# Performance work log

Hardware: AMD Instinct MI355X
Metric: run time of the kernel (lower is better)

The kernel has to match this reference:

```python
import jax, jax.numpy as jnp
import numpy as np

N_NODES = 1_000_000
MEM_DIM = 128
EDGE_DIM = 64
TIME_DIM = 16
N_EVENTS = 100_000
GRU_IN = 2 * MEM_DIM + EDGE_DIM + TIME_DIM  # 336


def setup_inputs() -> dict:
    key = jax.random.key(0)
    ks = jax.random.split(key, 16)
    sc = 0.05
    return {
        "memory": jax.random.normal(ks[0], (N_NODES, MEM_DIM), jnp.float32),
        "src": jax.random.randint(ks[1], (N_EVENTS,), 0, N_NODES, jnp.int32),
        "dst": jax.random.randint(ks[2], (N_EVENTS,), 0, N_NODES, jnp.int32),
        "ts": jax.random.uniform(ks[3], (N_EVENTS,), jnp.float32),
        "ef": jax.random.normal(ks[4], (N_EVENTS, EDGE_DIM), jnp.float32),
        # time_linear: Linear(1, 16)
        "W_time": jax.random.normal(ks[5], (TIME_DIM, 1), jnp.float32) * sc,
        "b_time": jax.random.normal(ks[6], (TIME_DIM,), jnp.float32) * sc,
        # GRUCell(336, 128): torch layout, gate order (r, z, n)
        "W_ih": jax.random.normal(ks[7], (3 * MEM_DIM, GRU_IN), jnp.float32) * sc,
        "W_hh": jax.random.normal(ks[8], (3 * MEM_DIM, MEM_DIM), jnp.float32) * sc,
        "b_ih": jax.random.normal(ks[9], (3 * MEM_DIM,), jnp.float32) * sc,
        "b_hh": jax.random.normal(ks[10], (3 * MEM_DIM,), jnp.float32) * sc,
        # predictor: Linear(256,128) -> ReLU -> Linear(128,1)
        "W_p1": jax.random.normal(ks[11], (MEM_DIM, 2 * MEM_DIM), jnp.float32) * sc,
        "b_p1": jax.random.normal(ks[12], (MEM_DIM,), jnp.float32) * sc,
        "W_p2": jax.random.normal(ks[13], (1, MEM_DIM), jnp.float32) * sc,
        "b_p2": jax.random.normal(ks[14], (1,), jnp.float32) * sc,
    }


def _gru_cell(x, h, W_ih, W_hh, b_ih, b_hh):
    gi = x @ W_ih.T + b_ih  # [E, 3H]
    gh = h @ W_hh.T + b_hh  # [E, 3H]
    i_r, i_z, i_n = jnp.split(gi, 3, axis=-1)
    h_r, h_z, h_n = jnp.split(gh, 3, axis=-1)
    r = jax.nn.sigmoid(i_r + h_r)
    z = jax.nn.sigmoid(i_z + h_z)
    n = jnp.tanh(i_n + r * h_n)
    return (1.0 - z) * n + z * h


def reference(memory, src, dst, ts, ef, W_time, b_time, W_ih, W_hh, b_ih, b_hh,
              W_p1, b_p1, W_p2, b_p2):
    # update_memory: gather -> time encode -> GRU -> scatter (dst write after src, matching torch)
    s = memory[src]  # [E, H]
    d = memory[dst]  # [E, H]
    te = jnp.sin(ts[:, None] @ W_time.T + b_time)  # [E, 16]
    inp = jnp.concatenate([s, d, ef, te], axis=-1)  # [E, 336]
    new_s = _gru_cell(inp, s, W_ih, W_hh, b_ih, b_hh)
    new_d = _gru_cell(inp, d, W_ih, W_hh, b_ih, b_hh)
    mem = memory.at[src].set(new_s).at[dst].set(new_d)
    # predict on updated memory
    h = jnp.concatenate([mem[src], mem[dst]], axis=-1)  # [E, 2H]
    pred = (jax.nn.relu(h @ W_p1.T + b_p1) @ W_p2.T + b_p2).squeeze(-1)  # [E]
    return pred, mem
```

## Files before the change

### kernel.cpp

```cpp
#include <hip/hip_runtime.h>
#include <hip/hip_bf16.h>
#include <math.h>

static constexpr int NN  = 1000000;
static constexpr int HD  = 128;
static constexpr int ED  = 64;
static constexpr int TD  = 16;
static constexpr int NE  = 100000;
static constexpr int GIN = 336;
static constexpr int KP  = 352;
static constexpr int KS  = KP / 32;
static constexpr int EB  = 32;
static constexpr int PS  = 264;
static constexpr int NBG = NE / EB;
static constexpr int NBC = 2 * NBG;
static constexpr int CR  = NN / NBC;
static constexpr int NIH = 24 * KS * 512;
static constexpr int NHH = 24 * 4 * 512;
static constexpr int NP1 = 8 * 8 * 512;
static constexpr int NBW = (NE + 511) / 512;
static constexpr int NBV = (NIH + NHH + NP1) / 512;

typedef __attribute__((ext_vector_type(8))) short bf16x8;
typedef __attribute__((ext_vector_type(4))) float f32x4;

__device__ inline unsigned f2bf(float x) {
    union { float f; unsigned u; } a; a.f = x;
    unsigned r = a.u + 0x7fff + ((a.u >> 16) & 1);
    return r >> 16;
}
__device__ inline float bf2f(unsigned short u) {
    union { unsigned u; float f; } a; a.u = ((unsigned)u) << 16; return a.f;
}
__device__ inline float fsig(float x) {
    return __builtin_amdgcn_rcpf(1.f + __builtin_amdgcn_exp2f(x * -1.44269504f));
}
__device__ inline float ftanh(float x) {
    return 1.f - 2.f * __builtin_amdgcn_rcpf(1.f + __builtin_amdgcn_exp2f(x * 2.88539008f));
}

__global__ void prio_kernel(const int* __restrict__ src, const int* __restrict__ dst,
                            int* __restrict__ prio) {
    int e = blockIdx.x * blockDim.x + threadIdx.x;
    if (e < NE) {
        atomicMax(&prio[src[e]], e);
        atomicMax(&prio[dst[e]], NE + e);
    }
}

__global__ __launch_bounds__(512) void prep_kernel(
    const float* __restrict__ memory,
    const int* __restrict__ src, const int* __restrict__ dst,
    const float* __restrict__ ts, const float* __restrict__ ef,
    const float* __restrict__ W_time, const float* __restrict__ b_time,
    const float* __restrict__ W_ih, const float* __restrict__ W_hh,
    const float* __restrict__ W_p1,
    const int* __restrict__ prio, unsigned char* __restrict__ win,
    unsigned short* __restrict__ A_pack,
    unsigned short* __restrict__ Wihf, unsigned short* __restrict__ Whhf,
    unsigned short* __restrict__ Wp1f,
    float* __restrict__ mem_out)
{
    const int bid = blockIdx.x;
    const int tid = threadIdx.x;

    if (bid < NBC + NBG) {
        if (bid % 3 != 2) {
            const int cb = (bid / 3) * 2 + (bid % 3);
            const float4* in4  = (const float4*)memory;
            float4*       out4 = (float4*)mem_out;
            const size_t base = (size_t)cb * CR * 32;
            for (int i = tid; i < CR * 32; i += 512)
                out4[base + i] = in4[base + i];
        } else {
            const int e0 = (bid / 3) * EB;
            for (int idx = tid; idx < EB * 88; idx += 512) {
                int e = idx / 88, c4 = idx % 88;
                float4 v = {0.f, 0.f, 0.f, 0.f};
                if (c4 < 32)      v = ((const float4*)&memory[(size_t)src[e0 + e] * HD])[c4];
                else if (c4 < 64) v = ((const float4*)&memory[(size_t)dst[e0 + e] * HD])[c4 - 32];
                else if (c4 < 80) v = ((const float4*)&ef[(size_t)(e0 + e) * ED])[c4 - 64];
                else if (c4 < 84) {
                    int j = (c4 - 80) * 4;
                    float t = ts[e0 + e];
                    v.x = __sinf(t * W_time[j]     + b_time[j]);
                    v.y = __sinf(t * W_time[j + 1] + b_time[j + 1]);
                    v.z = __sinf(t * W_time[j + 2] + b_time[j + 2]);
                    v.w = __sinf(t * W_time[j + 3] + b_time[j + 3]);
                }
                uint2 p;
                p.x = f2bf(v.x) | (f2bf(v.y) << 16);
                p.y = f2bf(v.z) | (f2bf(v.w) << 16);
                *(uint2*)&A_pack[(size_t)(e0 + e) * KP + c4 * 4] = p;
            }
        }
    } else if (bid < NBC + NBG + NBW) {
        int e = (bid - NBC - NBG) * 512 + tid;
        if (e < NE)
            win[e] = (unsigned char)((prio[src[e]] == e ? 1 : 0) |
                                     (prio[dst[e]] == NE + e ? 2 : 0));
    } else {
        int q = (bid - NBC - NBG - NBW) * 512 + tid;
        if (q < NIH) {
            int t = q / (KS * 512), rem = q % (KS * 512);
            int kk = rem / 512, li = rem % 512;
            int l = li >> 3, j = li & 7;
            int row = t * 16 + (l & 15);
            int col = kk * 32 + (l >> 4) * 8 + j;
            Wihf[q] = (col < GIN) ? (unsigned short)f2bf(W_ih[(size_t)row * GIN + col])
                                  : (unsigned short)0;
        } else if (q < NIH + NHH) {
            int p = q - NIH;
            int t = p / (4 * 512), rem = p % (4 * 512);
            int kk = rem / 512, li = rem % 512;
            int l = li >> 3, j = li & 7;
            int row = t * 16 + (l & 15);
            int col = kk * 32 + (l >> 4) * 8 + j;
            Whhf[p] = (unsigned short)f2bf(W_hh[(size_t)row * HD + col]);
        } else {
            int p = q - NIH - NHH;
            int w = p / (8 * 512), rem = p % (8 * 512);
            int kk = rem / 512, li = rem % 512;
            int l = li >> 3, j = li & 7;
            int row = w * 16 + (l & 15);
            int col = kk * 32 + (l >> 4) * 8 + j;
            Wp1f[p] = (unsigned short)f2bf(W_p1[(size_t)row * (2 * HD) + col]);
        }
    }
}

__global__ __launch_bounds__(512) void gru_kernel(
    const unsigned short* __restrict__ A_pack,
    const int* __restrict__ src, const int* __restrict__ dst,
    const unsigned short* __restrict__ Wihf, const unsigned short* __restrict__ Whhf,
    const float* __restrict__ b_ih, const float* __restrict__ b_hh,
    const unsigned char* __restrict__ win, float* __restrict__ mem_out)
{
    __shared__ unsigned short a_lds[EB * KP];
    const int tid = threadIdx.x;
    const int e0  = blockIdx.x * EB;

    {
        const uint4* g4 = (const uint4*)(A_pack + (size_t)e0 * KP);
        uint4* l4 = (uint4*)a_lds;
        for (int i = tid; i < EB * KP / 8; i += 512)
            l4[i] = g4[i];
    }
    __syncthreads();

    const int w    = tid >> 6;
    const int lane = tid & 63;
    const int lg   = lane >> 4;
    const int u    = w * 16 + (lane & 15);
    const int arow = lane & 15;

#define ALD(t, kkk) (*(const bf16x8*)&a_lds[(arow + (t) * 16) * KP + (kkk) * 32 + lg * 8])

    f32x4 z4 = {0.f, 0.f, 0.f, 0.f};
    f32x4 ir0 = z4, ir1 = z4, iz0 = z4, iz1 = z4, in0 = z4, in1 = z4;
    f32x4 sr0 = z4, sr1 = z4, sz0 = z4, sz1 = z4, sn0 = z4, sn1 = z4;
    f32x4 dr0 = z4, dr1 = z4, dz0 = z4, dz1 = z4, dn0 = z4, dn1 = z4;

#pragma unroll
    for (int kk = 0; kk < KS; ++kk) {
        bf16x8 b0 = *(const bf16x8*)&Wihf[(((size_t)(0 * 8 + w) * KS + kk) * 64 + lane) * 8];
        bf16x8 b1 = *(const bf16x8*)&Wihf[(((size_t)(1 * 8 + w) * KS + kk) * 64 + lane) * 8];
        bf16x8 b2 = *(const bf16x8*)&Wihf[(((size_t)(2 * 8 + w) * KS + kk) * 64 + lane) * 8];
        bf16x8 a0 = ALD(0, kk), a1 = ALD(1, kk);
        ir0 = __builtin_amdgcn_mfma_f32_16x16x32_bf16(a0, b0, ir0, 0, 0, 0);
        ir1 = __builtin_amdgcn_mfma_f32_16x16x32_bf16(a1, b0, ir1, 0, 0, 0);
        iz0 = __builtin_amdgcn_mfma_f32_16x16x32_bf16(a0, b1, iz0, 0, 0, 0);
        iz1 = __builtin_amdgcn_mfma_f32_16x16x32_bf16(a1, b1, iz1, 0, 0, 0);
        in0 = __builtin_amdgcn_mfma_f32_16x16x32_bf16(a0, b2, in0, 0, 0, 0);
        in1 = __builtin_amdgcn_mfma_f32_16x16x32_bf16(a1, b2, in1, 0, 0, 0);
    }
#pragma unroll
    for (int kk = 0; kk < 4; ++kk) {
        bf16x8 c0 = *(const bf16x8*)&Whhf[(((size_t)(0 * 8 + w) * 4 + kk) * 64 + lane) * 8];
        bf16x8 c1 = *(const bf16x8*)&Whhf[(((size_t)(1 * 8 + w) * 4 + kk) * 64 + lane) * 8];
        bf16x8 c2 = *(const bf16x8*)&Whhf[(((size_t)(2 * 8 + w) * 4 + kk) * 64 + lane) * 8];
        bf16x8 as0 = ALD(0, kk),     as1 = ALD(1, kk);
        bf16x8 ad0 = ALD(0, kk + 4), ad1 = ALD(1, kk + 4);
        sr0 = __builtin_amdgcn_mfma_f32_16x16x32_bf16(as0, c0, sr0, 0, 0, 0);
        sr1 = __builtin_amdgcn_mfma_f32_16x16x32_bf16(as1, c0, sr1, 0, 0, 0);
        dr0 = __builtin_amdgcn_mfma_f32_16x16x32_bf16(ad0, c0, dr0, 0, 0, 0);
        dr1 = __builtin_amdgcn_mfma_f32_16x16x32_bf16(ad1, c0, dr1, 0, 0, 0);
        sz0 = __builtin_amdgcn_mfma_f32_16x16x32_bf16(as0, c1, sz0, 0, 0, 0);
        sz1 = __builtin_amdgcn_mfma_f32_16x16x32_bf16(as1, c1, sz1, 0, 0, 0);
        dz0 = __builtin_amdgcn_mfma_f32_16x16x32_bf16(ad0, c1, dz0, 0, 0, 0);
        dz1 = __builtin_amdgcn_mfma_f32_16x16x32_bf16(ad1, c1, dz1, 0, 0, 0);
        sn0 = __builtin_amdgcn_mfma_f32_16x16x32_bf16(as0, c2, sn0, 0, 0, 0);
        sn1 = __builtin_amdgcn_mfma_f32_16x16x32_bf16(as1, c2, sn1, 0, 0, 0);
        dn0 = __builtin_amdgcn_mfma_f32_16x16x32_bf16(ad0, c2, dn0, 0, 0, 0);
        dn1 = __builtin_amdgcn_mfma_f32_16x16x32_bf16(ad1, c2, dn1, 0, 0, 0);
    }
#undef ALD

    const float bir = b_ih[u], biz = b_ih[u + 128], bin_ = b_ih[u + 256];
    const float bhr = b_hh[u], bhz = b_hh[u + 128], bhn = b_hh[u + 256];

    auto epilogue = [&](int t, f32x4 ir, f32x4 iz, f32x4 in_,
                        f32x4 sr, f32x4 sz, f32x4 sn,
                        f32x4 dr, f32x4 dz, f32x4 dn) {
#pragma unroll
        for (int j = 0; j < 4; ++j) {
            int el = t * 16 + lg * 4 + j, e = e0 + el;
            unsigned char wf = win[e];
            float gr_ = ir[j] + bir, gz_ = iz[j] + biz, gn_ = in_[j] + bin_;
            if (wf & 1) {
                float r = fsig(gr_ + sr[j] + bhr);
                float z = fsig(gz_ + sz[j] + bhz);
                float n = ftanh(gn_ + r * (sn[j] + bhn));
                float h = bf2f(a_lds[el * KP + u]);
                mem_out[(size_t)src[e] * HD + u] = (1.f - z) * n + z * h;
            }
            if (wf & 2) {
                float r = fsig(gr_ + dr[j] + bhr);
                float z = fsig(gz_ + dz[j] + bhz);
                float n = ftanh(gn_ + r * (dn[j] + bhn));
                float h = bf2f(a_lds[el * KP + 128 + u]);
                mem_out[(size_t)dst[e] * HD + u] = (1.f - z) * n + z * h;
            }
        }
    };
    epilogue(0, ir0, iz0, in0, sr0, sz0, sn0, dr0, dz0, dn0);
    epilogue(1, ir1, iz1, in1, sr1, sz1, sn1, dr1, dz1, dn1);
}

__global__ __launch_bounds__(512) void pred_kernel(
    const float* __restrict__ mem,
    const int* __restrict__ src, const int* __restrict__ dst,
    const unsigned short* __restrict__ Wp1f, const float* __restrict__ b_p1,
    const float* __restrict__ W_p2, const float* __restrict__ b_p2,
    float* __restrict__ pred)
{
    __shared__ unsigned short h_lds[32 * PS];
    __shared__ float partial[32][8];
    const int tid = threadIdx.x;
    const int e0  = blockIdx.x * 32;

    for (int idx = tid; idx < 32 * 64; idx += 512) {
        int e = idx >> 6, p = idx & 63;
        const float4* row = (p < 32) ? (const float4*)&mem[(size_t)src[e0 + e] * HD]
                                     : (const float4*)&mem[(size_t)dst[e0 + e] * HD];
        float4 v = row[p & 31];
        int col = (p < 32 ? 0 : 128) + (p & 31) * 4;
        uint2 q;
        q.x = f2bf(v.x) | (f2bf(v.y) << 16);
        q.y = f2bf(v.z) | (f2bf(v.w) << 16);
        *(uint2*)&h_lds[e * PS + col] = q;
    }
    __syncthreads();

    const int w    = tid >> 6;
    const int lane = tid & 63;
    const int lg   = lane >> 4;
    const int u    = w * 16 + (lane & 15);

    f32x4 p0 = {0.f, 0.f, 0.f, 0.f}, p1 = p0;
#pragma unroll
    for (int kk = 0; kk < 8; ++kk) {
        bf16x8 b  = *(const bf16x8*)&Wp1f[(((size_t)w * 8 + kk) * 64 + lane) * 8];
        bf16x8 a0 = *(const bf16x8*)&h_lds[(lane & 15) * PS + kk * 32 + lg * 8];
        bf16x8 a1 = *(const bf16x8*)&h_lds[((lane & 15) + 16) * PS + kk * 32 + lg * 8];
        p0 = __builtin_amdgcn_mfma_f32_16x16x32_bf16(a0, b, p0, 0, 0, 0);
        p1 = __builtin_amdgcn_mfma_f32_16x16x32_bf16(a1, b, p1, 0, 0, 0);
    }
    const float bp = b_p1[u], w2 = W_p2[u];

    auto reduce_tile = [&](int t, f32x4 acc) {
#pragma unroll
        for (int j = 0; j < 4; ++j) {
            float v = acc[j] + bp;
            v = (v > 0.f ? v : 0.f) * w2;
            v += __shfl_xor(v, 1, 64);
            v += __shfl_xor(v, 2, 64);
            v += __shfl_xor(v, 4, 64);
            v += __shfl_xor(v, 8, 64);
            if ((lane & 15) == 0) partial[t * 16 + lg * 4 + j][w] = v;
        }
    };
    reduce_tile(0, p0);
    reduce_tile(1, p1);
    __syncthreads();

    if (tid < 32) {
        float s = b_p2[0];
#pragma unroll
        for (int q = 0; q < 8; ++q) s += partial[tid][q];
        pred[e0 + tid] = s;
    }
}

extern "C" void kernel_launch(void* const* d_in, const int* in_sizes, int n_in,
                              void* d_out, int out_size, void* d_ws, size_t ws_size,
                              hipStream_t stream) {
    const float* memory = (const float*)d_in[0];
    const int*   src    = (const int*)d_in[1];
    const int*   dst    = (const int*)d_in[2];
    const float* ts     = (const float*)d_in[3];
    const float* ef     = (const float*)d_in[4];
    const float* W_time = (const float*)d_in[5];
    const float* b_time = (const float*)d_in[6];
    const float* W_ih   = (const float*)d_in[7];
    const float* W_hh   = (const float*)d_in[8];
    const float* b_ih   = (const float*)d_in[9];
    const float* b_hh   = (const float*)d_in[10];
    const float* W_p1   = (const float*)d_in[11];
    const float* b_p1   = (const float*)d_in[12];
    const float* W_p2   = (const float*)d_in[13];
    const float* b_p2   = (const float*)d_in[14];

    float* pred    = (float*)d_out;
    float* mem_out = pred + NE;

    char* ws = (char*)d_ws;
    int* prio            = (int*)ws;                ws += (size_t)NN * 4;
    unsigned short* Wihf = (unsigned short*)ws;     ws += (size_t)NIH * 2;
    unsigned short* Whhf = (unsigned short*)ws;     ws += (size_t)NHH * 2;
    unsigned short* Wp1f = (unsigned short*)ws;     ws += (size_t)NP1 * 2;
    unsigned char* win   = (unsigned char*)ws;      ws += 100352;
    unsigned short* A_pack = (unsigned short*)ws;

    hipMemsetAsync(prio, 0xFF, (size_t)NN * sizeof(int), stream);
    prio_kernel<<<(NE + 255) / 256, 256, 0, stream>>>(src, dst, prio);
    prep_kernel<<<NBC + NBG + NBW + NBV, 512, 0, stream>>>(
        memory, src, dst, ts, ef, W_time, b_time, W_ih, W_hh, W_p1,
        prio, win, A_pack, Wihf, Whhf, Wp1f, mem_out);
    gru_kernel<<<NBG, 512, 0, stream>>>(A_pack, src, dst, Wihf, Whhf,
                                        b_ih, b_hh, win, mem_out);
    pred_kernel<<<NE / 32, 512, 0, stream>>>(mem_out, src, dst,
                                             Wp1f, b_p1, W_p2, b_p2, pred);
}
```

Before: 392.4 us.

## Move memory copy into GRU kernel, skip rows that get overwritten

Moves the bulk memory-to-output copy from the pack kernel into the GRU kernel, interleaving copy blocks with GRU blocks so bandwidth-bound copying overlaps with MFMA compute. The copy now skips rows that events will overwrite, identified by their prio entry. The pack kernel becomes smaller and lets the GRU start sooner. s_setprio raises wave priority around the MFMA loops so GRU waves are favoured over the copy waves. The cost is an extra prio read per copied row and a higher block count in the fused kernel.

```diff
diff --git a/kernel.cpp b/kernel.cpp
--- a/kernel.cpp
+++ b/kernel.cpp
@@ -48,7 +48,7 @@
     }
 }
 
-__global__ __launch_bounds__(512) void prep_kernel(
+__global__ __launch_bounds__(512) void pack_kernel(
     const float* __restrict__ memory,
     const int* __restrict__ src, const int* __restrict__ dst,
     const float* __restrict__ ts, const float* __restrict__ ef,
@@ -58,49 +58,39 @@
     const int* __restrict__ prio, unsigned char* __restrict__ win,
     unsigned short* __restrict__ A_pack,
     unsigned short* __restrict__ Wihf, unsigned short* __restrict__ Whhf,
-    unsigned short* __restrict__ Wp1f,
-    float* __restrict__ mem_out)
+    unsigned short* __restrict__ Wp1f)
 {
     const int bid = blockIdx.x;
     const int tid = threadIdx.x;
 
-    if (bid < NBC + NBG) {
-        if (bid % 3 != 2) {
-            const int cb = (bid / 3) * 2 + (bid % 3);
-            const float4* in4  = (const float4*)memory;
-            float4*       out4 = (float4*)mem_out;
-            const size_t base = (size_t)cb * CR * 32;
-            for (int i = tid; i < CR * 32; i += 512)
-                out4[base + i] = in4[base + i];
-        } else {
-            const int e0 = (bid / 3) * EB;
-            for (int idx = tid; idx < EB * 88; idx += 512) {
-                int e = idx / 88, c4 = idx % 88;
-                float4 v = {0.f, 0.f, 0.f, 0.f};
-                if (c4 < 32)      v = ((const float4*)&memory[(size_t)src[e0 + e] * HD])[c4];
-                else if (c4 < 64) v = ((const float4*)&memory[(size_t)dst[e0 + e] * HD])[c4 - 32];
-                else if (c4 < 80) v = ((const float4*)&ef[(size_t)(e0 + e) * ED])[c4 - 64];
-                else if (c4 < 84) {
-                    int j = (c4 - 80) * 4;
-                    float t = ts[e0 + e];
-                    v.x = __sinf(t * W_time[j]     + b_time[j]);
-                    v.y = __sinf(t * W_time[j + 1] + b_time[j + 1]);
-                    v.z = __sinf(t * W_time[j + 2] + b_time[j + 2]);
-                    v.w = __sinf(t * W_time[j + 3] + b_time[j + 3]);
-                }
-                uint2 p;
-                p.x = f2bf(v.x) | (f2bf(v.y) << 16);
-                p.y = f2bf(v.z) | (f2bf(v.w) << 16);
-                *(uint2*)&A_pack[(size_t)(e0 + e) * KP + c4 * 4] = p;
+    if (bid < NBG) {
+        const int e0 = bid * EB;
+        for (int idx = tid; idx < EB * 88; idx += 512) {
+            int e = idx / 88, c4 = idx % 88;
+            float4 v = {0.f, 0.f, 0.f, 0.f};
+            if (c4 < 32)      v = ((const float4*)&memory[(size_t)src[e0 + e] * HD])[c4];
+            else if (c4 < 64) v = ((const float4*)&memory[(size_t)dst[e0 + e] * HD])[c4 - 32];
+            else if (c4 < 80) v = ((const float4*)&ef[(size_t)(e0 + e) * ED])[c4 - 64];
+            else if (c4 < 84) {
+                int j = (c4 - 80) * 4;
+                float t = ts[e0 + e];
+                v.x = __sinf(t * W_time[j]     + b_time[j]);
+                v.y = __sinf(t * W_time[j + 1] + b_time[j + 1]);
+                v.z = __sinf(t * W_time[j + 2] + b_time[j + 2]);
+                v.w = __sinf(t * W_time[j + 3] + b_time[j + 3]);
             }
-        }
-    } else if (bid < NBC + NBG + NBW) {
-        int e = (bid - NBC - NBG) * 512 + tid;
+            uint2 p;
+            p.x = f2bf(v.x) | (f2bf(v.y) << 16);
+            p.y = f2bf(v.z) | (f2bf(v.w) << 16);
+            *(uint2*)&A_pack[(size_t)(e0 + e) * KP + c4 * 4] = p;
+        }
+    } else if (bid < NBG + NBW) {
+        int e = (bid - NBG) * 512 + tid;
         if (e < NE)
             win[e] = (unsigned char)((prio[src[e]] == e ? 1 : 0) |
                                      (prio[dst[e]] == NE + e ? 2 : 0));
     } else {
-        int q = (bid - NBC - NBG - NBW) * 512 + tid;
+        int q = (bid - NBG - NBW) * 512 + tid;
         if (q < NIH) {
             int t = q / (KS * 512), rem = q % (KS * 512);
             int kk = rem / 512, li = rem % 512;
@@ -129,16 +119,33 @@
     }
 }
 
-__global__ __launch_bounds__(512) void gru_kernel(
+__global__ __launch_bounds__(512) void fat_kernel(
+    const float* __restrict__ memory,
     const unsigned short* __restrict__ A_pack,
     const int* __restrict__ src, const int* __restrict__ dst,
     const unsigned short* __restrict__ Wihf, const unsigned short* __restrict__ Whhf,
     const float* __restrict__ b_ih, const float* __restrict__ b_hh,
-    const unsigned char* __restrict__ win, float* __restrict__ mem_out)
+    const int* __restrict__ prio, const unsigned char* __restrict__ win,
+    float* __restrict__ mem_out)
 {
     __shared__ unsigned short a_lds[EB * KP];
+    const int bid = blockIdx.x;
     const int tid = threadIdx.x;
-    const int e0  = blockIdx.x * EB;
+
+    if (bid % 3 != 0) {
+        const int cb = bid - bid / 3 - 1;
+        const float4* in4  = (const float4*)memory;
+        float4*       out4 = (float4*)mem_out;
+        const int rbase = cb * CR;
+        for (int i = tid; i < CR * 32; i += 512) {
+            int r = rbase + (i >> 5);
+            if (prio[r] < 0)
+                out4[(size_t)r * 32 + (i & 31)] = in4[(size_t)r * 32 + (i & 31)];
+        }
+        return;
+    }
+
+    const int e0 = (bid / 3) * EB;
 
     {
         const uint4* g4 = (const uint4*)(A_pack + (size_t)e0 * KP);
@@ -161,6 +168,7 @@
     f32x4 sr0 = z4, sr1 = z4, sz0 = z4, sz1 = z4, sn0 = z4, sn1 = z4;
     f32x4 dr0 = z4, dr1 = z4, dz0 = z4, dz1 = z4, dn0 = z4, dn1 = z4;
 
+    __builtin_amdgcn_s_setprio(1);
 #pragma unroll
     for (int kk = 0; kk < KS; ++kk) {
         bf16x8 b0 = *(const bf16x8*)&Wihf[(((size_t)(0 * 8 + w) * KS + kk) * 64 + lane) * 8];
@@ -194,6 +202,7 @@
         dn0 = __builtin_amdgcn_mfma_f32_16x16x32_bf16(ad0, c2, dn0, 0, 0, 0);
         dn1 = __builtin_amdgcn_mfma_f32_16x16x32_bf16(ad1, c2, dn1, 0, 0, 0);
     }
+    __builtin_amdgcn_s_setprio(0);
 #undef ALD
 
     const float bir = b_ih[u], biz = b_ih[u + 128], bin_ = b_ih[u + 256];
@@ -324,11 +333,11 @@
 
     hipMemsetAsync(prio, 0xFF, (size_t)NN * sizeof(int), stream);
     prio_kernel<<<(NE + 255) / 256, 256, 0, stream>>>(src, dst, prio);
-    prep_kernel<<<NBC + NBG + NBW + NBV, 512, 0, stream>>>(
+    pack_kernel<<<NBG + NBW + NBV, 512, 0, stream>>>(
         memory, src, dst, ts, ef, W_time, b_time, W_ih, W_hh, W_p1,
-        prio, win, A_pack, Wihf, Whhf, Wp1f, mem_out);
-    gru_kernel<<<NBG, 512, 0, stream>>>(A_pack, src, dst, Wihf, Whhf,
-                                        b_ih, b_hh, win, mem_out);
+        prio, win, A_pack, Wihf, Whhf, Wp1f);
+    fat_kernel<<<NBG + NBC, 512, 0, stream>>>(
+        memory, A_pack, src, dst, Wihf, Whhf, b_ih, b_hh, prio, win, mem_out);
     pred_kernel<<<NE / 32, 512, 0, stream>>>(mem_out, src, dst,
                                              Wp1f, b_p1, W_p2, b_p2, pred);
 }
```

New measurement: 562.8 us. 43.4% more time.
